# Kernel optimization log

Measured on AMD Instinct MI355X. Metric: run time of the kernel, lower is better.

## Reference

```python
import jax, jax.numpy as jnp
import numpy as np

K1, K2, K3 = 6, 4, 3  # knn_graph k (loop=True -> self included, dist 0 is always top)


def _sqdist(a, b):
    # a: [B,N,3], b: [B,M,3] -> [B,N,M] squared euclidean distances
    an = jnp.sum(a * a, -1)[:, :, None]
    bn = jnp.sum(b * b, -1)[:, None, :]
    return an + bn - 2.0 * jnp.einsum('bnd,bmd->bnm', a, b)


def _knn_idx(pos, k):
    # for each point, indices of its k nearest neighbors (self included, loop=True)
    d = _sqdist(pos, pos)                 # [B,N,N]
    _, idx = jax.lax.top_k(-d, k)         # [B,N,k]
    return idx


def _gather(a, idx):
    # a: [B,N,...], idx: [B,...] -> per-cloud gather
    return jax.vmap(lambda ab, ib: ab[ib])(a, idx)


def _fps(pos, m):
    # farthest point sampling on one cloud [N,3], deterministic start at index 0
    min_d = jnp.sum((pos - pos[0]) ** 2, -1)  # [N]

    def step(min_d, _):
        idx = jnp.argmax(min_d)
        d = jnp.sum((pos - pos[idx]) ** 2, -1)
        return jnp.minimum(min_d, d), idx

    _, idxs = jax.lax.scan(step, min_d, None, length=m - 1)
    return jnp.concatenate([jnp.zeros((1,), dtype=idxs.dtype), idxs])


def _pn_layer(h, pos, k, W1, b1, W2, b2):
    # PointNetLayer: gather h_i/h_j/pos_i/pos_j over knn edges, MLP, max-aggregate
    idx = _knn_idx(pos, k)                       # [B,N,k]
    h_j = _gather(h, idx)                        # [B,N,k,C]
    pos_j = _gather(pos, idx)                    # [B,N,k,3]
    rel = pos_j - pos[:, :, None, :]             # pos_j - pos_i
    h_i = jnp.broadcast_to(h[:, :, None, :], h_j.shape)
    inp = jnp.concatenate([h_i, h_j, rel], -1)   # [B,N,k,2C+3]
    msg = jnp.maximum(inp @ W1 + b1, 0.0) @ W2 + b2
    return jnp.max(msg, axis=2)                  # scatter-max == dense max over k


def _forward(x, pos, W11, b11, W12, b12, W21, b21, W22, b22, W31, b31, W32, b32, Wr, br):
    h = jax.nn.relu(_pn_layer(x, pos, K1, W11, b11, W12, b12))
    idx = jax.vmap(lambda p: _fps(p, p.shape[0] // 2))(pos)   # ratio=0.5
    pos, h = _gather(pos, idx), _gather(h, idx)
    h = jax.nn.relu(_pn_layer(h, pos, K2, W21, b21, W22, b22))
    idx = jax.vmap(lambda p: _fps(p, p.shape[0] // 2))(pos)
    pos, h = _gather(pos, idx), _gather(h, idx)
    h = jax.nn.relu(_pn_layer(h, pos, K3, W31, b31, W32, b32))
    g = jnp.max(h, axis=1)                        # global_max_pool
    return g @ Wr + br                            # [B,10]


def _lin(key, fin, fout):
    k1, k2 = jax.random.split(key)
    lim = 1.0 / np.sqrt(fin)
    W = jax.random.uniform(k1, (fin, fout), minval=-lim, maxval=lim, dtype=jnp.float32)
    b = jax.random.uniform(k2, (fout,), minval=-lim, maxval=lim, dtype=jnp.float32)
    return W, b


def setup_inputs() -> dict:
    key = jax.random.key(0)
    ks = jax.random.split(key, 10)
    B, N = 16, 4096
    x = jax.random.normal(ks[0], (B, N, 1), dtype=jnp.float32)
    pos = jax.random.uniform(ks[1], (B, N, 3), dtype=jnp.float32)
    W11, b11 = _lin(ks[2], 1 * 2 + 3, 32)
    W12, b12 = _lin(ks[3], 32, 32)
    W21, b21 = _lin(ks[4], 32 * 2 + 3, 32)
    W22, b22 = _lin(ks[5], 32, 32)
    W31, b31 = _lin(ks[6], 32 * 2 + 3, 32)
    W32, b32 = _lin(ks[7], 32, 32)
    Wr, br = _lin(ks[8], 32, 10)
    return dict(x=x, pos=pos, W11=W11, b11=b11, W12=W12, b12=b12,
                W21=W21, b21=b21, W22=W22, b22=b22,
                W31=W31, b31=b31, W32=W32, b32=b32, Wr=Wr, br=br)


def reference(x, pos, W11, b11, W12, b12, W21, b21, W22, b22, W31, b31, W32, b32, Wr, br):
    return _forward(x, pos, W11, b11, W12, b12, W21, b21, W22, b22,
                    W31, b31, W32, b32, Wr, br)
```

## Files before the change

### kernel.cpp

```cpp
#include <hip/hip_runtime.h>

#define BATCH 16
#define NP1 4096
#define NP2 2048
#define NP3 1024

typedef float v2f __attribute__((ext_vector_type(2)));

__device__ __forceinline__ float f_add(float a, float b) { return __fadd_rn(a, b); }
__device__ __forceinline__ float f_mul(float a, float b) { return __fmul_rn(a, b); }
__device__ __forceinline__ float f_sub(float a, float b) { return __fsub_rn(a, b); }
__device__ __forceinline__ float sqnorm3(float x, float y, float z) {
  return f_add(f_add(f_mul(x, x), f_mul(y, y)), f_mul(z, z));
}

__device__ __forceinline__ unsigned long long u64max(unsigned long long a,
                                                     unsigned long long b) {
  return a > b ? a : b;
}
__device__ __forceinline__ unsigned long long u64min(unsigned long long a,
                                                     unsigned long long b) {
  return a < b ? a : b;
}
__device__ __forceinline__ double dmax(double a, double b) { return __builtin_fmax(a, b); }
__device__ __forceinline__ double dmin(double a, double b) { return __builtin_fmin(a, b); }

template<int CTRL, int RMASK>
__device__ __forceinline__ unsigned long long dpp_u64(unsigned long long k) {
  const int lo = __builtin_amdgcn_update_dpp(0, (int)(unsigned)k, CTRL, RMASK, 0xF, true);
  const int hi = __builtin_amdgcn_update_dpp(0, (int)(unsigned)(k >> 32), CTRL, RMASK, 0xF, true);
  return ((unsigned long long)(unsigned)hi << 32) | (unsigned)lo;
}
template<int CTRL, int RMASK>
__device__ __forceinline__ double dpp_dbl(double v) {
  return __longlong_as_double(
      (long long)dpp_u64<CTRL, RMASK>((unsigned long long)__double_as_longlong(v)));
}


__device__ __forceinline__ void tup_comb(double& a1, double& a2, double b1, double b2) {
  const double hi = dmax(a1, b1);
  const double lo = dmin(a1, b1);
  a2 = dmax(lo, dmax(a2, b2));
  a1 = hi;
}
template<int CTRL, int RMASK>
__device__ __forceinline__ void tup_stage(double& a1, double& a2) {
  const double b1 = dpp_dbl<CTRL, RMASK>(a1);
  const double b2 = dpp_dbl<CTRL, RMASK>(a2);
  tup_comb(a1, a2, b1, b2);
}

template<int N, int M>
__device__ void fps_block(char* __restrict__ smem, const float* __restrict__ P,
                          int* __restrict__ samp, float* __restrict__ pos_out)
{
#pragma clang fp contract(off)
  constexpr int THREADS = 512;
  constexpr int E = N / THREADS;
  constexpr int P2 = E / 2;
  float4* pos4 = (float4*)smem;
  unsigned short* ord = (unsigned short*)(smem + 16 * N);
  int* sampL = (int*)(smem + 18 * N);
  unsigned* cursor = (unsigned*)(smem + 18 * N + 4 * M);
  double* kslots = (double*)(smem + 18 * N + 4 * M + 32);
  const int tid = threadIdx.x;
  const int lane = tid & 63, wv = tid >> 6;
  const int myslot = lane & 7;
  if (tid < 8) cursor[tid] = 0u;
  __syncthreads();
  int oct[E];
#pragma unroll
  for (int e = 0; e < E; ++e) {
    const int t = e * THREADS + tid;
    const float x = P[t * 3], y = P[t * 3 + 1], z = P[t * 3 + 2];
    pos4[t] = make_float4(x, y, z, 0.f);
    oct[e] = (x > 0.5f ? 1 : 0) | (y > 0.5f ? 2 : 0) | (z > 0.5f ? 4 : 0);
    atomicAdd(&cursor[oct[e]], 1u);
  }
  __syncthreads();
  if (tid == 0) {
    unsigned run = 0;
#pragma unroll
    for (int o = 0; o < 8; ++o) { const unsigned c = cursor[o]; cursor[o] = run; run += c; }
  }
  __syncthreads();
#pragma unroll
  for (int e = 0; e < E; ++e) {
    const unsigned d = atomicAdd(&cursor[oct[e]], 1u);
    ord[d] = (unsigned short)(e * THREADS + tid);
  }
  __syncthreads();
  const float4 p0 = pos4[0];
  const float x0 = p0.x, y0 = p0.y, z0 = p0.z;
  v2f X2[P2], Y2[P2], Z2[P2], MD2[P2];
  unsigned ILO[E];
  float mnx = 1e30f, mny = 1e30f, mnz = 1e30f;
  float mxx = -1e30f, mxy = -1e30f, mxz = -1e30f;
  {
    const v2f x0v = {x0, x0}, y0v = {y0, y0}, z0v = {z0, z0};
#pragma unroll
    for (int p = 0; p < P2; ++p) {
      const int q0 = wv * (64 * E) + (2 * p) * 64 + lane;
      const int o0 = ord[q0], o1 = ord[q0 + 64];
      const float4 a0 = pos4[o0], a1 = pos4[o1];
      X2[p] = (v2f){a0.x, a1.x}; Y2[p] = (v2f){a0.y, a1.y}; Z2[p] = (v2f){a0.z, a1.z};
      mnx = fminf(mnx, fminf(a0.x, a1.x)); mxx = fmaxf(mxx, fmaxf(a0.x, a1.x));
      mny = fminf(mny, fminf(a0.y, a1.y)); mxy = fmaxf(mxy, fmaxf(a0.y, a1.y));
      mnz = fminf(mnz, fminf(a0.z, a1.z)); mxz = fmaxf(mxz, fmaxf(a0.z, a1.z));
      const v2f dx = X2[p] - x0v, dy = Y2[p] - y0v, dz = Z2[p] - z0v;
      MD2[p] = (dx * dx + dy * dy) + dz * dz;
      ILO[2 * p]     = 0xFFFFFFFFu - (unsigned)o0;
      ILO[2 * p + 1] = 0xFFFFFFFFu - (unsigned)o1;
    }
  }
#pragma unroll
  for (int off = 1; off < 64; off <<= 1) {
    mnx = fminf(mnx, __shfl_xor(mnx, off)); mxx = fmaxf(mxx, __shfl_xor(mxx, off));
    mny = fminf(mny, __shfl_xor(mny, off)); mxy = fmaxf(mxy, __shfl_xor(mxy, off));
    mnz = fminf(mnz, __shfl_xor(mnz, off)); mxz = fmaxf(mxz, __shfl_xor(mxz, off));
  }
  if (tid == 0) sampL[0] = 0;
  bool dirty = true;
  double W1 = 0.0, W2 = 0.0;
  int s = 1, it = 0;
#pragma unroll 1
  while (s < M) {
    if (dirty) {
      double k[E];
#pragma unroll
      for (int p = 0; p < P2; ++p) {
        k[2 * p] = __longlong_as_double((long long)(
            ((unsigned long long)__float_as_uint(MD2[p].x) << 32) | ILO[2 * p]));
        k[2 * p + 1] = __longlong_as_double((long long)(
            ((unsigned long long)__float_as_uint(MD2[p].y) << 32) | ILO[2 * p + 1]));
      }
      double A1 = dmax(k[0], k[1]), A2 = dmin(k[0], k[1]);
      double B1 = dmax(k[2], k[3]), B2 = dmin(k[2], k[3]);
      double C1 = dmax(k[4], k[5]), C2 = dmin(k[4], k[5]);
      double D1 = dmax(k[6], k[7]), D2 = dmin(k[6], k[7]);
      tup_comb(A1, A2, B1, B2); tup_comb(C1, C2, D1, D2); tup_comb(A1, A2, C1, C2);
      tup_stage<0x111, 0xF>(A1, A2);
      tup_stage<0x112, 0xF>(A1, A2);
      tup_stage<0x114, 0xF>(A1, A2);
      tup_stage<0x118, 0xF>(A1, A2);
      tup_stage<0x142, 0xA>(A1, A2);
      tup_stage<0x143, 0xC>(A1, A2);
      W1 = A1; W2 = A2;
    }
    const int pb = it & 1;
    if (lane == 63) ((double2*)kslots)[pb * 8 + wv] = make_double2(W1, W2);
    __syncthreads();
    const double2 tt = ((double2*)kslots)[pb * 8 + myslot];
    const double2 tn = ((double2*)kslots)[pb * 8 + (myslot ^ 1)];
    double T1 = tt.x, T2 = tt.y;
    tup_comb(T1, T2, tn.x, tn.y);
    tup_stage<0x4E, 0xF>(T1, T2);
    tup_stage<0x124, 0xF>(T1, T2);
    const unsigned long long g1b = (unsigned long long)__double_as_longlong(T1);
    const unsigned long long g2b = (unsigned long long)__double_as_longlong(T2);
    const int gi1 = (int)(0xFFFFFFFFu - (unsigned)g1b);
    const int gi2 = (int)(0xFFFFFFFFu - (unsigned)g2b);
    const float4 sp1 = pos4[gi1];
    const float4 sp2 = pos4[gi2];
    const float md2b = __uint_as_float((unsigned)(g2b >> 32));
    const float ddx = f_sub(sp2.x, sp1.x), ddy = f_sub(sp2.y, sp1.y),
                ddz = f_sub(sp2.z, sp1.z);
    const float dchk = f_add(f_add(f_mul(ddx, ddx), f_mul(ddy, ddy)), f_mul(ddz, ddz));
    const bool take2 = (s + 1 < M) && (dchk >= md2b);
    if (tid == 0) { sampL[s] = gi1; if (take2) sampL[s + 1] = gi2; }
    const float wmaxf = __uint_as_float((unsigned)__builtin_amdgcn_readlane(
        (int)(unsigned)((unsigned long long)__double_as_longlong(W1) >> 32), 63));
    const float m1x = fmaxf(fmaxf(f_sub(mnx, sp1.x), f_sub(sp1.x, mxx)), 0.f);
    const float m1y = fmaxf(fmaxf(f_sub(mny, sp1.y), f_sub(sp1.y, mxy)), 0.f);
    const float m1z = fmaxf(fmaxf(f_sub(mnz, sp1.z), f_sub(sp1.z, mxz)), 0.f);
    const bool u1 = sqnorm3(m1x, m1y, m1z) < wmaxf;
    const float m2x = fmaxf(fmaxf(f_sub(mnx, sp2.x), f_sub(sp2.x, mxx)), 0.f);
    const float m2y = fmaxf(fmaxf(f_sub(mny, sp2.y), f_sub(sp2.y, mxy)), 0.f);
    const float m2z = fmaxf(fmaxf(f_sub(mnz, sp2.z), f_sub(sp2.z, mxz)), 0.f);
    const bool u2 = take2 && (sqnorm3(m2x, m2y, m2z) < wmaxf);
    if (u1 | u2) {
      dirty = true;
      if (u1 & u2) {
        const v2f s1x = {sp1.x, sp1.x}, s1y = {sp1.y, sp1.y}, s1z = {sp1.z, sp1.z};
        const v2f s2x = {sp2.x, sp2.x}, s2y = {sp2.y, sp2.y}, s2z = {sp2.z, sp2.z};
#pragma unroll
        for (int p = 0; p < P2; ++p) {
          const v2f dx1 = X2[p] - s1x, dy1 = Y2[p] - s1y, dz1 = Z2[p] - s1z;
          const v2f d1 = (dx1 * dx1 + dy1 * dy1) + dz1 * dz1;
          MD2[p] = __builtin_elementwise_min(MD2[p], d1);
          const v2f dx2 = X2[p] - s2x, dy2 = Y2[p] - s2y, dz2 = Z2[p] - s2z;
          const v2f d2 = (dx2 * dx2 + dy2 * dy2) + dz2 * dz2;
          MD2[p] = __builtin_elementwise_min(MD2[p], d2);
        }
      } else {
        const float4 sp = u1 ? sp1 : sp2;
        const v2f sxv = {sp.x, sp.x}, syv = {sp.y, sp.y}, szv = {sp.z, sp.z};
#pragma unroll
        for (int p = 0; p < P2; ++p) {
          const v2f dx = X2[p] - sxv, dy = Y2[p] - syv, dz = Z2[p] - szv;
          const v2f d = (dx * dx + dy * dy) + dz * dz;
          MD2[p] = __builtin_elementwise_min(MD2[p], d);
        }
      }
    } else {
      dirty = false;
    }
    s += take2 ? 2 : 1;
    ++it;
  }
  __syncthreads();
  for (int s2 = tid; s2 < M; s2 += THREADS) {
    const int g = sampL[s2];
    samp[s2] = g;
    const float4 sp2 = pos4[g];
    pos_out[3 * s2 + 0] = sp2.x;
    pos_out[3 * s2 + 1] = sp2.y;
    pos_out[3 * s2 + 2] = sp2.z;
  }
}

__device__ __forceinline__ float f4c(const float4& v, int c) {
  return c == 0 ? v.x : c == 1 ? v.y : c == 2 ? v.z : v.w;
}
__device__ __forceinline__ void fma4(float4& a, float v, const float4& w) {
  a.x += v * w.x; a.y += v * w.y; a.z += v * w.z; a.w += v * w.w;
}

template<int K, int C>
__device__ void pn_compute(
    const float4* __restrict__ sW1, const float4* __restrict__ sW2,
    const float* __restrict__ sb1, const float* __restrict__ sb2,
    const float* __restrict__ P, const float* __restrict__ Hsrc,
    const int* __restrict__ hmap, int i, float xi, float yi, float zi,
    const int* kn, float* __restrict__ outrow)
{
  float4 abase[8];
#pragma unroll
  for (int o = 0; o < 8; ++o)
    abase[o] = make_float4(sb1[4 * o], sb1[4 * o + 1], sb1[4 * o + 2], sb1[4 * o + 3]);
  if constexpr (C == 1) {
    const float v = Hsrc[hmap ? hmap[i] : i];
#pragma unroll
    for (int o = 0; o < 8; ++o) fma4(abase[o], v, sW1[o]);
  } else {
    const int ri = hmap ? hmap[i] : i;
    const float4* Hi = (const float4*)(Hsrc + (size_t)ri * C);
#pragma unroll
    for (int c4 = 0; c4 < C / 4; ++c4) {
      const float4 hv = Hi[c4];
#pragma unroll
      for (int q = 0; q < 4; ++q) {
        const float v = f4c(hv, q);
#pragma unroll
        for (int o = 0; o < 8; ++o) fma4(abase[o], v, sW1[(4 * c4 + q) * 8 + o]);
      }
    }
  }
  float4 best[8];
#pragma unroll
  for (int o = 0; o < 8; ++o)
    best[o] = make_float4(-__builtin_inff(), -__builtin_inff(), -__builtin_inff(), -__builtin_inff());

  auto edge_pair = [&](int j0, int j1) {
    float4 a0[8], a1[8];
#pragma unroll
    for (int o = 0; o < 8; ++o) { a0[o] = abase[o]; a1[o] = abase[o]; }
    const float rx0 = P[j0 * 3] - xi, ry0 = P[j0 * 3 + 1] - yi, rz0 = P[j0 * 3 + 2] - zi;
    const float rx1 = P[j1 * 3] - xi, ry1 = P[j1 * 3 + 1] - yi, rz1 = P[j1 * 3 + 2] - zi;
    if constexpr (C == 1) {
      const float v0 = Hsrc[hmap ? hmap[j0] : j0], v1 = Hsrc[hmap ? hmap[j1] : j1];
#pragma unroll
      for (int o = 0; o < 8; ++o) {
        const float4 w = sW1[C * 8 + o];
        fma4(a0[o], v0, w); fma4(a1[o], v1, w);
      }
    } else {
      const int r0i = hmap ? hmap[j0] : j0, r1i = hmap ? hmap[j1] : j1;
      const float4* Hj0 = (const float4*)(Hsrc + (size_t)r0i * C);
      const float4* Hj1 = (const float4*)(Hsrc + (size_t)r1i * C);
#pragma unroll
      for (int c4 = 0; c4 < C / 4; ++c4) {
        const float4 h0 = Hj0[c4], h1 = Hj1[c4];
#pragma unroll
        for (int q = 0; q < 4; ++q) {
          const float v0 = f4c(h0, q), v1 = f4c(h1, q);
#pragma unroll
          for (int o = 0; o < 8; ++o) {
            const float4 w = sW1[(C + 4 * c4 + q) * 8 + o];
            fma4(a0[o], v0, w); fma4(a1[o], v1, w);
          }
        }
      }
    }
    const float r0[3] = {rx0, ry0, rz0}, r1[3] = {rx1, ry1, rz1};
#pragma unroll
    for (int r = 0; r < 3; ++r) {
#pragma unroll
      for (int o = 0; o < 8; ++o) {
        const float4 w = sW1[(2 * C + r) * 8 + o];
        fma4(a0[o], r0[r], w); fma4(a1[o], r1[r], w);
      }
    }
#pragma unroll
    for (int o = 0; o < 8; ++o) {
      a0[o].x = fmaxf(a0[o].x, 0.f); a0[o].y = fmaxf(a0[o].y, 0.f);
      a0[o].z = fmaxf(a0[o].z, 0.f); a0[o].w = fmaxf(a0[o].w, 0.f);
      a1[o].x = fmaxf(a1[o].x, 0.f); a1[o].y = fmaxf(a1[o].y, 0.f);
      a1[o].z = fmaxf(a1[o].z, 0.f); a1[o].w = fmaxf(a1[o].w, 0.f);
    }
#pragma unroll
    for (int hf = 0; hf < 2; ++hf) {
      float4 m0[4], m1[4];
#pragma unroll
      for (int o4 = 0; o4 < 4; ++o4) {
        const int c0 = 16 * hf + 4 * o4;
        m0[o4] = make_float4(sb2[c0], sb2[c0 + 1], sb2[c0 + 2], sb2[c0 + 3]);
        m1[o4] = m0[o4];
      }
#pragma unroll
      for (int c = 0; c < 32; ++c) {
        const float v0 = f4c(a0[c >> 2], c & 3), v1 = f4c(a1[c >> 2], c & 3);
#pragma unroll
        for (int o4 = 0; o4 < 4; ++o4) {
          const float4 w = sW2[c * 8 + hf * 4 + o4];
          fma4(m0[o4], v0, w); fma4(m1[o4], v1, w);
        }
      }
#pragma unroll
      for (int o4 = 0; o4 < 4; ++o4) {
        float4& bb = best[hf * 4 + o4];
        bb.x = fmaxf(bb.x, fmaxf(m0[o4].x, m1[o4].x));
        bb.y = fmaxf(bb.y, fmaxf(m0[o4].y, m1[o4].y));
        bb.z = fmaxf(bb.z, fmaxf(m0[o4].z, m1[o4].z));
        bb.w = fmaxf(bb.w, fmaxf(m0[o4].w, m1[o4].w));
      }
    }
  };

#pragma unroll
  for (int e = 0; e + 1 < K; e += 2) edge_pair(kn[e], kn[e + 1]);

  float4* ho = (float4*)outrow;
#pragma unroll
  for (int o = 0; o < 8; ++o)
    ho[o] = make_float4(fmaxf(best[o].x, 0.0f), fmaxf(best[o].y, 0.0f),
                        fmaxf(best[o].z, 0.0f), fmaxf(best[o].w, 0.0f));
}

template<int K, int NC, int C, int THREADS>
__device__ void fused_knn_pn(char* __restrict__ smem,
    const float* __restrict__ P, const float* __restrict__ Hsrc,
    const int* __restrict__ hmap,
    const float* __restrict__ W1, const float* __restrict__ b1,
    const float* __restrict__ W2, const float* __restrict__ b2,
    float* __restrict__ hout, int s)
{
  constexpr int CIN = 2 * C + 3;
  float4* tile = (float4*)smem;
  float4* sW1 = (float4*)(smem + 16 * 1024);
  float4* sW2 = sW1 + CIN * 8;
  float* sb1 = (float*)(sW2 + 32 * 8);
  float* sb2 = sb1 + 32;
  const int tid = threadIdx.x;
  for (int t = tid; t < CIN * 8; t += THREADS) sW1[t] = ((const float4*)W1)[t];
  for (int t = tid; t < 32 * 8; t += THREADS) sW2[t] = ((const float4*)W2)[t];
  if (tid < 32) { sb1[tid] = b1[tid]; sb2[tid] = b2[tid]; }

  const float xi = P[s * 3], yi = P[s * 3 + 1], zi = P[s * 3 + 2];
  const float ni = sqnorm3(xi, yi, zi);
  float bd[K]; int bj[K];
#pragma unroll
  for (int t = 0; t < K; ++t) { bd[t] = __builtin_inff(); bj[t] = 0; }
  for (int base = 0; base < NC; base += 1024) {
    __syncthreads();
    for (int t = tid; t < 1024; t += THREADS) {
      const float* q = P + (size_t)(base + t) * 3;
      const float x = q[0], y = q[1], z = q[2];
      tile[t] = make_float4(x, y, z, sqnorm3(x, y, z));
    }
    __syncthreads();
#pragma unroll 1
    for (int t = 0; t < 1024; t += 8) {
      float dv[8];
#pragma unroll
      for (int u = 0; u < 8; ++u) {
        const float4 q = tile[t + u];
        const float dot = f_add(f_add(f_mul(xi, q.x), f_mul(yi, q.y)), f_mul(zi, q.z));
        dv[u] = f_sub(f_add(ni, q.w), f_mul(2.0f, dot));
      }
#pragma unroll
      for (int u = 0; u < 8; ++u) {
        if (dv[u] < bd[K - 1]) {
          bd[K - 1] = dv[u]; bj[K - 1] = base + t + u;
#pragma unroll
          for (int r = K - 1; r > 0; --r) {
            if (bd[r] < bd[r - 1]) {
              float td = bd[r]; bd[r] = bd[r - 1]; bd[r - 1] = td;
              int   tj = bj[r]; bj[r] = bj[r - 1]; bj[r - 1] = tj;
            } else break;
          }
        }
      }
    }
  }
  pn_compute<K, C>(sW1, sW2, sb1, sb2, P, Hsrc, hmap, s, xi, yi, zi, bj,
                   hout + (size_t)s * 32);
}

template<int K, int NC>
__device__ void fused_knn_pn_quad(char* __restrict__ smem,
    const float* __restrict__ P, const float* __restrict__ Hsrc,
    const int* __restrict__ hmap,
    const float* __restrict__ W1, const float* __restrict__ b1,
    const float* __restrict__ W2, const float* __restrict__ b2,
    float* __restrict__ hout, int s, int q)
{
  constexpr int THREADS = 256;
  constexpr int RQ = NC / 4;
  constexpr int CIN = 67;
  float4* tile = (float4*)smem;
  float4* sW1 = (float4*)(smem + 16 * (NC + 4));
  float4* sW2 = sW1 + CIN * 8;
  float* sb1 = (float*)(sW2 + 32 * 8);
  float* sb2 = sb1 + 32;
  const int tid = threadIdx.x;

  for (int t = tid; t < NC; t += THREADS) {
    const float* c = P + (size_t)t * 3;
    const float x = c[0], y = c[1], z = c[2];
    tile[t + t / RQ] = make_float4(x, y, z, sqnorm3(x, y, z));
  }
  for (int t = tid; t < CIN * 8; t += THREADS) sW1[t] = ((const float4*)W1)[t];
  for (int t = tid; t < 32 * 8; t += THREADS) sW2[t] = ((const float4*)W2)[t];
  if (tid < 32) { sb1[tid] = b1[tid]; sb2[tid] = b2[tid]; }
  __syncthreads();

  const float4 qv = tile[s + s / RQ];
  const float xi = qv.x, yi = qv.y, zi = qv.z, ni = qv.w;

  const int ri = hmap ? hmap[s] : s;
  float4 hi4[8];
  {
    const float4* Hi = (const float4*)(Hsrc + (size_t)ri * 32);
#pragma unroll
    for (int c4 = 0; c4 < 8; ++c4) hi4[c4] = Hi[c4];
  }

  float bd[4]; int bj[4];
#pragma unroll
  for (int t = 0; t < 4; ++t) { bd[t] = __builtin_inff(); bj[t] = 0; }
  const int sbase = q * (RQ + 1);
#pragma unroll 1
  for (int t = 0; t < RQ; t += 8) {
    float dv[8];
#pragma unroll
    for (int u = 0; u < 8; ++u) {
      const float4 c = tile[sbase + t + u];
      const float dot = f_add(f_add(f_mul(xi, c.x), f_mul(yi, c.y)), f_mul(zi, c.z));
      dv[u] = f_sub(f_add(ni, c.w), f_mul(2.0f, dot));
    }
#pragma unroll
    for (int u = 0; u < 8; ++u) {
      if (dv[u] < bd[3]) {
        bd[3] = dv[u]; bj[3] = q * RQ + t + u;
#pragma unroll
        for (int r = 3; r > 0; --r) {
          if (bd[r] < bd[r - 1]) {
            float td = bd[r]; bd[r] = bd[r - 1]; bd[r - 1] = td;
            int   tj = bj[r]; bj[r] = bj[r - 1]; bj[r - 1] = tj;
          } else break;
        }
      }
    }
  }
  unsigned long long a0, a1, a2, a3;
  {
    auto mk = [](float d, int j) {
      unsigned u = __float_as_uint(d);
      u ^= (unsigned)((int)u >> 31) | 0x80000000u;
      return ((unsigned long long)u << 32) | (unsigned)j;
    };
    a0 = mk(bd[0], bj[0]); a1 = mk(bd[1], bj[1]);
    a2 = mk(bd[2], bj[2]); a3 = mk(bd[3], bj[3]);
  }
  {
    const unsigned long long b0 = __shfl_xor(a0, 1), b1_ = __shfl_xor(a1, 1),
                             b2_ = __shfl_xor(a2, 1), b3_ = __shfl_xor(a3, 1);
    const unsigned long long t0 = u64min(a0, b3_), t1 = u64min(a1, b2_),
                             t2 = u64min(a2, b1_), t3 = u64min(a3, b0);
    const unsigned long long u0 = u64min(t0, t2), u2 = u64max(t0, t2),
                             u1 = u64min(t1, t3), u3 = u64max(t1, t3);
    a0 = u64min(u0, u1); a1 = u64max(u0, u1);
    a2 = u64min(u2, u3); a3 = u64max(u2, u3);
  }
  {
    const unsigned long long b0 = __shfl_xor(a0, 2), b1_ = __shfl_xor(a1, 2),
                             b2_ = __shfl_xor(a2, 2), b3_ = __shfl_xor(a3, 2);
    const unsigned long long t0 = u64min(a0, b3_), t1 = u64min(a1, b2_),
                             t2 = u64min(a2, b1_), t3 = u64min(a3, b0);
    const unsigned long long u0 = u64min(t0, t2), u2 = u64max(t0, t2),
                             u1 = u64min(t1, t3), u3 = u64max(t1, t3);
    a0 = u64min(u0, u1); a1 = u64max(u0, u1);
    a2 = u64min(u2, u3); a3 = u64max(u2, u3);
  }
  const int e = (q < K) ? q : (K - 1);
  const unsigned long long ke = (e == 0) ? a0 : (e == 1) ? a1 : (e == 2) ? a2 : a3;
  const int jn = (int)(unsigned)ke;

  const int rj = hmap ? hmap[jn] : jn;
  float4 hj4[8];
  {
    const float4* Hj = (const float4*)(Hsrc + (size_t)rj * 32);
#pragma unroll
    for (int c4 = 0; c4 < 8; ++c4) hj4[c4] = Hj[c4];
  }
  float4 acc[8];
#pragma unroll
  for (int o = 0; o < 8; ++o)
    acc[o] = make_float4(sb1[4 * o], sb1[4 * o + 1], sb1[4 * o + 2], sb1[4 * o + 3]);
#pragma unroll
  for (int c4 = 0; c4 < 8; ++c4) {
    const float4 hv = hi4[c4];
#pragma unroll
    for (int t = 0; t < 4; ++t) {
      const float v = f4c(hv, t);
#pragma unroll
      for (int o = 0; o < 8; ++o) fma4(acc[o], v, sW1[(4 * c4 + t) * 8 + o]);
    }
  }
#pragma unroll
  for (int c4 = 0; c4 < 8; ++c4) {
    const float4 hv = hj4[c4];
#pragma unroll
    for (int t = 0; t < 4; ++t) {
      const float v = f4c(hv, t);
#pragma unroll
      for (int o = 0; o < 8; ++o) fma4(acc[o], v, sW1[(32 + 4 * c4 + t) * 8 + o]);
    }
  }
  const float4 cj = tile[jn + jn / RQ];
  const float r3[3] = {cj.x - xi, cj.y - yi, cj.z - zi};
#pragma unroll
  for (int r = 0; r < 3; ++r)
#pragma unroll
    for (int o = 0; o < 8; ++o) fma4(acc[o], r3[r], sW1[(64 + r) * 8 + o]);
#pragma unroll
  for (int o = 0; o < 8; ++o) {
    acc[o].x = fmaxf(acc[o].x, 0.f); acc[o].y = fmaxf(acc[o].y, 0.f);
    acc[o].z = fmaxf(acc[o].z, 0.f); acc[o].w = fmaxf(acc[o].w, 0.f);
  }
  float4 m[8];
#pragma unroll
  for (int o = 0; o < 8; ++o)
    m[o] = make_float4(sb2[4 * o], sb2[4 * o + 1], sb2[4 * o + 2], sb2[4 * o + 3]);
#pragma unroll
  for (int c = 0; c < 32; ++c) {
    const float v = f4c(acc[c >> 2], c & 3);
#pragma unroll
    for (int o = 0; o < 8; ++o) fma4(m[o], v, sW2[c * 8 + o]);
  }
#pragma unroll
  for (int o = 0; o < 8; ++o) {
    float4 v = m[o];
    v.x = fmaxf(v.x, __shfl_xor(v.x, 1)); v.y = fmaxf(v.y, __shfl_xor(v.y, 1));
    v.z = fmaxf(v.z, __shfl_xor(v.z, 1)); v.w = fmaxf(v.w, __shfl_xor(v.w, 1));
    v.x = fmaxf(v.x, __shfl_xor(v.x, 2)); v.y = fmaxf(v.y, __shfl_xor(v.y, 2));
    v.z = fmaxf(v.z, __shfl_xor(v.z, 2)); v.w = fmaxf(v.w, __shfl_xor(v.w, 2));
    m[o] = v;
  }
  float4* ho = (float4*)(hout + (size_t)s * 32);
  {
    const float4 v0 = m[2 * q], v1 = m[2 * q + 1];
    ho[2 * q] = make_float4(fmaxf(v0.x, 0.f), fmaxf(v0.y, 0.f),
                            fmaxf(v0.z, 0.f), fmaxf(v0.w, 0.f));
    ho[2 * q + 1] = make_float4(fmaxf(v1.x, 0.f), fmaxf(v1.y, 0.f),
                                fmaxf(v1.z, 0.f), fmaxf(v1.w, 0.f));
  }
}

__global__ __launch_bounds__(512) void megaA(
    const float* __restrict__ x, const float* __restrict__ pos,
    const float* __restrict__ W11, const float* __restrict__ b11,
    const float* __restrict__ W12, const float* __restrict__ b12,
    int* __restrict__ samp1, float* __restrict__ pos2, float* __restrict__ h1full)
{
  __shared__ __align__(16) char smem[82240];
  if (blockIdx.x < BATCH) {
    const int b = blockIdx.x;
    fps_block<NP1, NP2>(smem, pos + (size_t)b * NP1 * 3, samp1 + b * NP2,
                        pos2 + (size_t)b * NP2 * 3);
  } else {
    const int id = blockIdx.x - BATCH;
    const int b = id >> 3;
    const int s = (id & 7) * 512 + threadIdx.x;
    fused_knn_pn<6, NP1, 1, 512>(smem, pos + (size_t)b * NP1 * 3, x + (size_t)b * NP1,
                                 nullptr, W11, b11, W12, b12,
                                 h1full + (size_t)b * NP1 * 32, s);
  }
}

__global__ __launch_bounds__(256) void megaB(
    const float* __restrict__ pos2, const int* __restrict__ samp1,
    const float* __restrict__ h1full,
    const float* __restrict__ W21, const float* __restrict__ b21,
    const float* __restrict__ W22, const float* __restrict__ b22,
    float* __restrict__ h2out)
{
  __shared__ __align__(16) char smem[(2048 + 4) * 16 + 67 * 8 * 16 + 32 * 8 * 16 + 256];
  const int b = blockIdx.x >> 4;
  const int s = ((blockIdx.x & 15) << 6) + (threadIdx.x >> 2);
  const int q = threadIdx.x & 3;
  fused_knn_pn_quad<4, NP2>(smem, pos2 + (size_t)b * NP2 * 3,
                            h1full + (size_t)b * NP1 * 32, samp1 + b * NP2,
                            W21, b21, W22, b22, h2out + (size_t)b * NP3 * 32, s, q);
}

__global__ __launch_bounds__(256) void megaC(
    const float* __restrict__ pos2, const float* __restrict__ h2out,
    const float* __restrict__ W31, const float* __restrict__ b31,
    const float* __restrict__ W32, const float* __restrict__ b32,
    float* __restrict__ h3full)
{
  __shared__ __align__(16) char smem[(1024 + 4) * 16 + 67 * 8 * 16 + 32 * 8 * 16 + 256];
  const int b = blockIdx.x >> 4;
  const int s = ((blockIdx.x & 15) << 6) + (threadIdx.x >> 2);
  const int q = threadIdx.x & 3;
  fused_knn_pn_quad<3, NP3>(smem, pos2 + (size_t)b * NP2 * 3,
                            h2out + (size_t)b * NP3 * 32, nullptr,
                            W31, b31, W32, b32, h3full + (size_t)b * NP3 * 32, s, q);
}

__global__ __launch_bounds__(256) void final_kernel(
    const float* __restrict__ h, const float* __restrict__ Wr,
    const float* __restrict__ br, float* __restrict__ out)
{
  __shared__ float red[8][32];
  __shared__ float g[32];
  const int b = blockIdx.x;
  const int c = threadIdx.x & 31, grp = threadIdx.x >> 5;
  const float* H = h + (size_t)b * NP3 * 32;
  float m = -__builtin_inff();
  for (int r = grp; r < NP3; r += 8) m = fmaxf(m, H[r * 32 + c]);
  red[grp][c] = m;
  __syncthreads();
  if (threadIdx.x < 32) {
    float v = red[0][c];
#pragma unroll
    for (int w = 1; w < 8; ++w) v = fmaxf(v, red[w][c]);
    g[c] = v;
  }
  __syncthreads();
  if (threadIdx.x < 10) {
    float v = br[threadIdx.x];
#pragma unroll
    for (int cc = 0; cc < 32; ++cc) v += g[cc] * Wr[cc * 10 + threadIdx.x];
    out[b * 10 + threadIdx.x] = v;
  }
}

extern "C" void kernel_launch(void* const* d_in, const int* in_sizes, int n_in,
                              void* d_out, int out_size, void* d_ws, size_t ws_size,
                              hipStream_t stream) {
  const float* x   = (const float*)d_in[0];
  const float* pos = (const float*)d_in[1];
  const float* W11 = (const float*)d_in[2];
  const float* b11 = (const float*)d_in[3];
  const float* W12 = (const float*)d_in[4];
  const float* b12 = (const float*)d_in[5];
  const float* W21 = (const float*)d_in[6];
  const float* b21 = (const float*)d_in[7];
  const float* W22 = (const float*)d_in[8];
  const float* b22 = (const float*)d_in[9];
  const float* W31 = (const float*)d_in[10];
  const float* b31 = (const float*)d_in[11];
  const float* W32 = (const float*)d_in[12];
  const float* b32 = (const float*)d_in[13];
  const float* Wr  = (const float*)d_in[14];
  const float* br  = (const float*)d_in[15];
  float* out = (float*)d_out;

  char* p = (char*)d_ws;
  auto alloc = [&](size_t bytes) {
    char* r = p; p += (bytes + 255) & ~(size_t)255; return r;
  };
  int*   samp1  = (int*)  alloc(sizeof(int)   * BATCH * NP2);
  float* pos2   = (float*)alloc(sizeof(float) * BATCH * NP2 * 3);
  float* h1full = (float*)alloc(sizeof(float) * BATCH * NP1 * 32);
  float* h2out  = (float*)alloc(sizeof(float) * BATCH * NP3 * 32);
  float* h3full = (float*)alloc(sizeof(float) * BATCH * NP3 * 32);

  megaA<<<BATCH + BATCH * (NP1 / 512), 512, 0, stream>>>(
      x, pos, W11, b11, W12, b12, samp1, pos2, h1full);
  megaB<<<BATCH * 16, 256, 0, stream>>>(
      pos2, samp1, h1full, W21, b21, W22, b22, h2out);
  megaC<<<BATCH * 16, 256, 0, stream>>>(
      pos2, h2out, W31, b31, W32, b32, h3full);
  final_kernel<<<BATCH, 256, 0, stream>>>(h3full, Wr, br, out);
}
```

Measured before the change: 1.291 ms.

## Split each query point's kNN+MLP across eight lanes instead of four

Stages B and C now assign eight threads per query point rather than four. Each thread scans one eighth of the candidate tile and the partial top-k lists are merged in an extra shuffle round. Each lane still evaluates one neighbor's MLP, but lanes with q>=4 duplicate the work of lanes q&3. Grids double to 512 blocks, which gives more parallelism in the distance scan on a 256-CU device, at the cost of redundant MLP work, an extra merge stage, and twice the per-block tile loads and weight staging.

Measured after the change: 1.321 ms. 1.02x slower.

```diff
diff --git a/kernel.cpp b/kernel.cpp
--- a/kernel.cpp
+++ b/kernel.cpp
@@ -409,7 +409,7 @@
 }
 
 template<int K, int NC>
-__device__ void fused_knn_pn_quad(char* __restrict__ smem,
+__device__ void fused_knn_pn_oct(char* __restrict__ smem,
     const float* __restrict__ P, const float* __restrict__ Hsrc,
     const int* __restrict__ hmap,
     const float* __restrict__ W1, const float* __restrict__ b1,
@@ -417,10 +417,10 @@
     float* __restrict__ hout, int s, int q)
 {
   constexpr int THREADS = 256;
-  constexpr int RQ = NC / 4;
+  constexpr int RQ = NC / 8;
   constexpr int CIN = 67;
   float4* tile = (float4*)smem;
-  float4* sW1 = (float4*)(smem + 16 * (NC + 4));
+  float4* sW1 = (float4*)(smem + 16 * (NC + 8));
   float4* sW2 = sW1 + CIN * 8;
   float* sb1 = (float*)(sW2 + 32 * 8);
   float* sb2 = sb1 + 32;
@@ -484,9 +484,10 @@
     a0 = mk(bd[0], bj[0]); a1 = mk(bd[1], bj[1]);
     a2 = mk(bd[2], bj[2]); a3 = mk(bd[3], bj[3]);
   }
-  {
-    const unsigned long long b0 = __shfl_xor(a0, 1), b1_ = __shfl_xor(a1, 1),
-                             b2_ = __shfl_xor(a2, 1), b3_ = __shfl_xor(a3, 1);
+#pragma unroll
+  for (int st = 1; st <= 4; st <<= 1) {
+    const unsigned long long b0 = __shfl_xor(a0, st), b1_ = __shfl_xor(a1, st),
+                             b2_ = __shfl_xor(a2, st), b3_ = __shfl_xor(a3, st);
     const unsigned long long t0 = u64min(a0, b3_), t1 = u64min(a1, b2_),
                              t2 = u64min(a2, b1_), t3 = u64min(a3, b0);
     const unsigned long long u0 = u64min(t0, t2), u2 = u64max(t0, t2),
@@ -494,17 +495,8 @@
     a0 = u64min(u0, u1); a1 = u64max(u0, u1);
     a2 = u64min(u2, u3); a3 = u64max(u2, u3);
   }
-  {
-    const unsigned long long b0 = __shfl_xor(a0, 2), b1_ = __shfl_xor(a1, 2),
-                             b2_ = __shfl_xor(a2, 2), b3_ = __shfl_xor(a3, 2);
-    const unsigned long long t0 = u64min(a0, b3_), t1 = u64min(a1, b2_),
-                             t2 = u64min(a2, b1_), t3 = u64min(a3, b0);
-    const unsigned long long u0 = u64min(t0, t2), u2 = u64max(t0, t2),
-                             u1 = u64min(t1, t3), u3 = u64max(t1, t3);
-    a0 = u64min(u0, u1); a1 = u64max(u0, u1);
-    a2 = u64min(u2, u3); a3 = u64max(u2, u3);
-  }
-  const int e = (q < K) ? q : (K - 1);
+  const int eq = q & 3;
+  const int e = (eq < K) ? eq : (K - 1);
   const unsigned long long ke = (e == 0) ? a0 : (e == 1) ? a1 : (e == 2) ? a2 : a3;
   const int jn = (int)(unsigned)ke;
 
@@ -563,19 +555,18 @@
 #pragma unroll
   for (int o = 0; o < 8; ++o) {
     float4 v = m[o];
-    v.x = fmaxf(v.x, __shfl_xor(v.x, 1)); v.y = fmaxf(v.y, __shfl_xor(v.y, 1));
-    v.z = fmaxf(v.z, __shfl_xor(v.z, 1)); v.w = fmaxf(v.w, __shfl_xor(v.w, 1));
-    v.x = fmaxf(v.x, __shfl_xor(v.x, 2)); v.y = fmaxf(v.y, __shfl_xor(v.y, 2));
-    v.z = fmaxf(v.z, __shfl_xor(v.z, 2)); v.w = fmaxf(v.w, __shfl_xor(v.w, 2));
+#pragma unroll
+    for (int st = 1; st <= 4; st <<= 1) {
+      v.x = fmaxf(v.x, __shfl_xor(v.x, st)); v.y = fmaxf(v.y, __shfl_xor(v.y, st));
+      v.z = fmaxf(v.z, __shfl_xor(v.z, st)); v.w = fmaxf(v.w, __shfl_xor(v.w, st));
+    }
     m[o] = v;
   }
   float4* ho = (float4*)(hout + (size_t)s * 32);
   {
-    const float4 v0 = m[2 * q], v1 = m[2 * q + 1];
-    ho[2 * q] = make_float4(fmaxf(v0.x, 0.f), fmaxf(v0.y, 0.f),
-                            fmaxf(v0.z, 0.f), fmaxf(v0.w, 0.f));
-    ho[2 * q + 1] = make_float4(fmaxf(v1.x, 0.f), fmaxf(v1.y, 0.f),
-                                fmaxf(v1.z, 0.f), fmaxf(v1.w, 0.f));
+    const float4 v0 = m[q];
+    ho[q] = make_float4(fmaxf(v0.x, 0.f), fmaxf(v0.y, 0.f),
+                        fmaxf(v0.z, 0.f), fmaxf(v0.w, 0.f));
   }
 }
 
@@ -607,13 +598,13 @@
     const float* __restrict__ W22, const float* __restrict__ b22,
     float* __restrict__ h2out)
 {
-  __shared__ __align__(16) char smem[(2048 + 4) * 16 + 67 * 8 * 16 + 32 * 8 * 16 + 256];
-  const int b = blockIdx.x >> 4;
-  const int s = ((blockIdx.x & 15) << 6) + (threadIdx.x >> 2);
-  const int q = threadIdx.x & 3;
-  fused_knn_pn_quad<4, NP2>(smem, pos2 + (size_t)b * NP2 * 3,
-                            h1full + (size_t)b * NP1 * 32, samp1 + b * NP2,
-                            W21, b21, W22, b22, h2out + (size_t)b * NP3 * 32, s, q);
+  __shared__ __align__(16) char smem[(2048 + 8) * 16 + 67 * 8 * 16 + 32 * 8 * 16 + 256];
+  const int b = blockIdx.x >> 5;
+  const int s = ((blockIdx.x & 31) << 5) + (threadIdx.x >> 3);
+  const int q = threadIdx.x & 7;
+  fused_knn_pn_oct<4, NP2>(smem, pos2 + (size_t)b * NP2 * 3,
+                           h1full + (size_t)b * NP1 * 32, samp1 + b * NP2,
+                           W21, b21, W22, b22, h2out + (size_t)b * NP3 * 32, s, q);
 }
 
 __global__ __launch_bounds__(256) void megaC(
@@ -622,13 +613,13 @@
     const float* __restrict__ W32, const float* __restrict__ b32,
     float* __restrict__ h3full)
 {
-  __shared__ __align__(16) char smem[(1024 + 4) * 16 + 67 * 8 * 16 + 32 * 8 * 16 + 256];
-  const int b = blockIdx.x >> 4;
-  const int s = ((blockIdx.x & 15) << 6) + (threadIdx.x >> 2);
-  const int q = threadIdx.x & 3;
-  fused_knn_pn_quad<3, NP3>(smem, pos2 + (size_t)b * NP2 * 3,
-                            h2out + (size_t)b * NP3 * 32, nullptr,
-                            W31, b31, W32, b32, h3full + (size_t)b * NP3 * 32, s, q);
+  __shared__ __align__(16) char smem[(1024 + 8) * 16 + 67 * 8 * 16 + 32 * 8 * 16 + 256];
+  const int b = blockIdx.x >> 5;
+  const int s = ((blockIdx.x & 31) << 5) + (threadIdx.x >> 3);
+  const int q = threadIdx.x & 7;
+  fused_knn_pn_oct<3, NP3>(smem, pos2 + (size_t)b * NP2 * 3,
+                           h2out + (size_t)b * NP3 * 32, nullptr,
+                           W31, b31, W32, b32, h3full + (size_t)b * NP3 * 32, s, q);
 }
 
 __global__ __launch_bounds__(256) void final_kernel(
@@ -692,9 +683,9 @@
 
   megaA<<<BATCH + BATCH * (NP1 / 512), 512, 0, stream>>>(
       x, pos, W11, b11, W12, b12, samp1, pos2, h1full);
-  megaB<<<BATCH * 16, 256, 0, stream>>>(
+  megaB<<<BATCH * 32, 256, 0, stream>>>(
       pos2, samp1, h1full, W21, b21, W22, b22, h2out);
-  megaC<<<BATCH * 16, 256, 0, stream>>>(
+  megaC<<<BATCH * 32, 256, 0, stream>>>(
       pos2, h2out, W31, b31, W32, b32, h3full);
   final_kernel<<<BATCH, 256, 0, stream>>>(h3full, Wr, br, out);
 }
```
